# Kernel optimization log

Measured on AMD Instinct MI355X. Metric: run time of the kernel, lower is better.

The kernel has to match this reference:

```python
import jax, jax.numpy as jnp
import numpy as np

N_GRAPHS = 8
NODES_PER_G = 1024
EDGES_PER_G = 2048
N = N_GRAPHS * NODES_PER_G          # 8192 nodes
E = N_GRAPHS * EDGES_PER_G          # 16384 edges
IN_DIM, EDGE_DIM, HID, OUT_DIM, T = 10, 9, 64, 3, 5
EPS = 1e-6


def _lin(key, fan_in, fan_out):
    kw, kb = jax.random.split(key)
    s = 1.0 / np.sqrt(fan_in)
    return (jax.random.uniform(kw, (fan_in, fan_out), jnp.float32, -s, s),
            jax.random.uniform(kb, (fan_out,), jnp.float32, -s, s))


def setup_inputs() -> dict:
    key = jax.random.key(0)
    ks = jax.random.split(key, 32)
    x = jax.random.normal(ks[0], (N, IN_DIM), jnp.float32)
    edge_attr = jax.random.normal(ks[1], (E, EDGE_DIM), jnp.float32)
    # edges stay within their own graph (block structure)
    src_l = jax.random.randint(ks[2], (E,), 0, NODES_PER_G)
    dst_l = jax.random.randint(ks[3], (E,), 0, NODES_PER_G)
    off = jnp.repeat(jnp.arange(N_GRAPHS, dtype=jnp.int64) * NODES_PER_G, EDGES_PER_G)
    edge_index = jnp.stack([src_l.astype(jnp.int64) + off, dst_l.astype(jnp.int64) + off])
    batch = jnp.repeat(jnp.arange(N_GRAPHS, dtype=jnp.int64), NODES_PER_G)

    lift_w1, lift_b1 = _lin(ks[4], IN_DIM, HID)
    lift_w2, lift_b2 = _lin(ks[5], HID, HID)
    proj_w1, proj_b1 = _lin(ks[6], HID, HID)
    proj_w2, proj_b2 = _lin(ks[7], HID, OUT_DIM)

    def stackp(fn, base):
        ws, bs = zip(*[fn(ks[base + t]) for t in range(T)])
        return jnp.stack(ws), jnp.stack(bs)

    root_w, root_b = stackp(lambda k: _lin(k, HID, HID), 8)
    k_w1, k_b1 = stackp(lambda k: _lin(k, EDGE_DIM, HID), 13)
    k_w2, k_b2 = stackp(lambda k: _lin(k, HID, HID), 18)
    k_w3, k_b3 = stackp(lambda k: _lin(k, HID, HID * HID), 23)

    return dict(x=x, edge_attr=edge_attr,
                lift_w1=lift_w1, lift_b1=lift_b1, lift_w2=lift_w2, lift_b2=lift_b2,
                root_w=root_w, root_b=root_b,
                k_w1=k_w1, k_b1=k_b1, k_w2=k_w2, k_b2=k_b2, k_w3=k_w3, k_b3=k_b3,
                proj_w1=proj_w1, proj_b1=proj_b1, proj_w2=proj_w2, proj_b2=proj_b2,
                edge_index=edge_index, batch=batch)


def reference(x, edge_attr, lift_w1, lift_b1, lift_w2, lift_b2,
              root_w, root_b, k_w1, k_b1, k_w2, k_b2, k_w3, k_b3,
              proj_w1, proj_b1, proj_w2, proj_b2, edge_index, batch):
    src, dst = edge_index[0], edge_index[1]

    # --- per-graph edge_attr standardization (scatter mean/std over each graph's edges) ---
    eb = batch[src]                                           # graph id per edge [E]
    ones_e = jnp.ones((E,), jnp.float32)
    cnt = jax.ops.segment_sum(ones_e, eb, num_segments=N_GRAPHS)          # [G]
    mean = jax.ops.segment_sum(edge_attr, eb, num_segments=N_GRAPHS) / cnt[:, None]
    msq = jax.ops.segment_sum(edge_attr * edge_attr, eb, num_segments=N_GRAPHS) / cnt[:, None]
    std = jnp.sqrt(jnp.clip(msq - mean * mean, 0.0))
    ea = (edge_attr - mean[eb]) / (std[eb] + EPS)             # [E, edge_dim]

    # --- lift MLP ---
    v = jax.nn.relu(x @ lift_w1 + lift_b1) @ lift_w2 + lift_b2  # [N, HID]

    # --- T kernel layers: v' = relu(W_root v + mean_{j->i} K(e_ij) v_j) ---
    deg = jnp.clip(jax.ops.segment_sum(ones_e, dst, num_segments=N), 1.0)  # [N]
    for t in range(T):
        h = jax.nn.relu(ea @ k_w1[t] + k_b1[t])
        h = jax.nn.relu(h @ k_w2[t] + k_b2[t])
        ker = (h @ k_w3[t] + k_b3[t]).reshape(E, HID, HID)    # per-edge 64x64 kernel
        msg = jnp.einsum('eij,ej->ei', ker, v[src])           # [E, HID]
        aggr = jax.ops.segment_sum(msg, dst, num_segments=N) / deg[:, None]
        v = jax.nn.relu(v @ root_w[t] + root_b[t] + aggr)
        # dropout (p=0.1) is identity in eval mode

    # --- project MLP ---
    return jax.nn.relu(v @ proj_w1 + proj_b1) @ proj_w2 + proj_b2  # [N, OUT_DIM]
```

## Files before the change

### kernel.cpp

```cpp
#include <hip/hip_runtime.h>

#define N_GRAPHS    8
#define EDGES_PER_G 2048
#define NN          8192
#define EE          16384
#define IN_DIM      10
#define EDGE_DIM    9
#define HID         64
#define OUT_DIM     3
#define TT          5
#define EPSN        1e-6f

typedef float f32x4 __attribute__((ext_vector_type(4)));
typedef short bf16x8s __attribute__((ext_vector_type(8)));

union BF8 { __bf16 h[8]; bf16x8s v; };

__device__ inline void edgemlp16(int e0, int tid,
    const float* __restrict__ ear, const float* __restrict__ meanb,
    const float* __restrict__ invstd,
    const float* __restrict__ w1, const float* __restrict__ b1,
    const float* __restrict__ w2, const float* __restrict__ b2,
    float* smem, float* __restrict__ h2T) {
  float (*sh)[68] = (float (*)[68])smem;
  float (*st)[68] = (float (*)[68])(smem + 16 * 68);
  int g = tid >> 6, lane = tid & 63;
  int eb = e0 + g * 4;
  int gg = e0 >> 11;
  const float* mb = meanb + gg * EDGE_DIM;
  const float* is = invstd + gg * EDGE_DIM;
  float xn[4][EDGE_DIM];
#pragma unroll
  for (int k = 0; k < 4; ++k) {
    const float* er = ear + (size_t)(eb + k) * EDGE_DIM;
#pragma unroll
    for (int d = 0; d < EDGE_DIM; ++d) xn[k][d] = (er[d] - mb[d]) * is[d];
  }
  float a0 = b1[lane], a1 = a0, a2 = a0, a3 = a0;
#pragma unroll
  for (int d = 0; d < EDGE_DIM; ++d) {
    float w = w1[d * HID + lane];
    a0 += xn[0][d] * w; a1 += xn[1][d] * w;
    a2 += xn[2][d] * w; a3 += xn[3][d] * w;
  }
  sh[g * 4 + 0][lane] = fmaxf(a0, 0.f);
  sh[g * 4 + 1][lane] = fmaxf(a1, 0.f);
  sh[g * 4 + 2][lane] = fmaxf(a2, 0.f);
  sh[g * 4 + 3][lane] = fmaxf(a3, 0.f);
  __syncthreads();
  float o0 = b2[lane], o1 = o0, o2 = o0, o3 = o0;
#pragma unroll
  for (int h = 0; h < HID; ++h) {
    float w = w2[h * HID + lane];
    o0 += sh[g * 4 + 0][h] * w; o1 += sh[g * 4 + 1][h] * w;
    o2 += sh[g * 4 + 2][h] * w; o3 += sh[g * 4 + 3][h] * w;
  }
  st[g * 4 + 0][lane] = fmaxf(o0, 0.f);
  st[g * 4 + 1][lane] = fmaxf(o1, 0.f);
  st[g * 4 + 2][lane] = fmaxf(o2, 0.f);
  st[g * 4 + 3][lane] = fmaxf(o3, 0.f);
  __syncthreads();
  for (int i = tid; i < HID * 16; i += 256) {
    int c = i >> 4, eo = i & 15;
    h2T[(size_t)c * EE + e0 + eo] = st[eo][c];
  }
}

__global__ __launch_bounds__(256) void k_stats(
    const float* __restrict__ ear, float* __restrict__ meanb,
    float* __restrict__ invstd, float* __restrict__ degf) {
  __shared__ float sw[4][2 * EDGE_DIM];
  int b = blockIdx.x;
  int g = threadIdx.x >> 6, lane = threadIdx.x & 63;
  if (b < N_GRAPHS) {
    int gg = b;
    float ls[EDGE_DIM], lq[EDGE_DIM];
#pragma unroll
    for (int d = 0; d < EDGE_DIM; ++d) { ls[d] = 0.f; lq[d] = 0.f; }
    for (int e = threadIdx.x; e < EDGES_PER_G; e += blockDim.x) {
      const float* row = ear + (size_t)(gg * EDGES_PER_G + e) * EDGE_DIM;
#pragma unroll
      for (int d = 0; d < EDGE_DIM; ++d) { float xv = row[d]; ls[d] += xv; lq[d] += xv * xv; }
    }
#pragma unroll
    for (int d = 0; d < EDGE_DIM; ++d) {
#pragma unroll
      for (int off = 32; off > 0; off >>= 1) {
        ls[d] += __shfl_down(ls[d], off);
        lq[d] += __shfl_down(lq[d], off);
      }
    }
    if (lane == 0) {
#pragma unroll
      for (int d = 0; d < EDGE_DIM; ++d) {
        sw[g][d] = ls[d];
        sw[g][EDGE_DIM + d] = lq[d];
      }
    }
    __syncthreads();
    if (threadIdx.x < EDGE_DIM) {
      int d = threadIdx.x;
      float s0 = sw[0][d] + sw[1][d] + sw[2][d] + sw[3][d];
      float q0 = sw[0][EDGE_DIM + d] + sw[1][EDGE_DIM + d] +
                 sw[2][EDGE_DIM + d] + sw[3][EDGE_DIM + d];
      float m  = s0 * (1.0f / EDGES_PER_G);
      float mq = q0 * (1.0f / EDGES_PER_G);
      float var = fmaxf(mq - m * m, 0.f);
      meanb[gg * EDGE_DIM + d]  = m;
      invstd[gg * EDGE_DIM + d] = 1.f / (sqrtf(var) + EPSN);
    }
  } else {
    int idx = (b - N_GRAPHS) * 256 + threadIdx.x;
    ((float4*)degf)[idx] = make_float4(0.f, 0.f, 0.f, 0.f);
  }
}

#define PRE_EM0   (EE / 16)
#define PRE_LIFT  (NN / 4)
#define PRE_BPREP 1024
#define PRE_DEG   (EE / 256)
#define PRE_ZAG   (NN * HID / 1024)
__global__ __launch_bounds__(256) void k_pre(
    const float* __restrict__ x,
    const float* __restrict__ lw1, const float* __restrict__ lb1,
    const float* __restrict__ lw2, const float* __restrict__ lb2,
    float* __restrict__ v,
    const float* __restrict__ kw3, const float* __restrict__ kb3,
    unsigned short* __restrict__ Bbf,
    const int* __restrict__ dst, float* __restrict__ degf,
    const float* __restrict__ ear, const float* __restrict__ meanb,
    const float* __restrict__ invstd, float* __restrict__ aggr,
    const float* __restrict__ w1, const float* __restrict__ b1,
    const float* __restrict__ w2, const float* __restrict__ b2,
    float* __restrict__ h2T0) {
  __shared__ float smem[2 * 16 * 68];
  int b = blockIdx.x;
  int g = threadIdx.x >> 6, lane = threadIdx.x & 63;
  if (b < PRE_EM0) {
    edgemlp16(b * 16, threadIdx.x, ear, meanb, invstd, w1, b1, w2, b2,
              smem, h2T0);
  } else if (b < PRE_EM0 + PRE_LIFT) {
    float (*sh)[HID] = (float (*)[HID])smem;
    int n = (b - PRE_EM0) * 4 + g;
    const float* xr = x + n * IN_DIM;
    float a = lb1[lane];
#pragma unroll
    for (int d = 0; d < IN_DIM; ++d) a += xr[d] * lw1[d * HID + lane];
    sh[g][lane] = fmaxf(a, 0.f);
    __syncthreads();
    float o = lb2[lane];
#pragma unroll
    for (int h = 0; h < HID; ++h) o += sh[g][h] * lw2[h * HID + lane];
    v[n * HID + lane] = o;
  } else if (b < PRE_EM0 + PRE_LIFT + PRE_BPREP) {
    const int total = TT * 65 * 4096;
    for (int i = (b - (PRE_EM0 + PRE_LIFT)) * 256 + (int)threadIdx.x; i < total;
         i += PRE_BPREP * 256) {
      int xx   = i & 4095;
      int call = i >> 12;
      int t = call / 65;
      int c = call - t * 65;
      int sn = xx >> 9;
      int s  = sn >> 2, nt = sn & 3;
      int l9 = xx & 511;
      int ln = l9 >> 3, jj = l9 & 7;
      int nn15 = ln & 15, qq = ln >> 4;
      int x_in = (nt * 16 + nn15) * 64 + s * 32 + qq * 8 + jj;
      float val = (c < 64) ? kw3[(size_t)(t * 64 + c) * 4096 + x_in]
                           : kb3[(size_t)t * 4096 + x_in];
      union { __bf16 h; unsigned short s16; } u;
      u.h = (__bf16)val;
      Bbf[i] = u.s16;
    }
  } else if (b < PRE_EM0 + PRE_LIFT + PRE_BPREP + PRE_DEG) {
    int e = (b - (PRE_EM0 + PRE_LIFT + PRE_BPREP)) * 256 + threadIdx.x;
    atomicAdd(&degf[dst[e]], 1.f);
  } else {
    int idx = (b - (PRE_EM0 + PRE_LIFT + PRE_BPREP + PRE_DEG)) * 256 + threadIdx.x;
    ((float4*)aggr)[idx] = make_float4(0.f, 0.f, 0.f, 0.f);
  }
}

__global__ __launch_bounds__(256) void k_msg(const float* __restrict__ v,
    const float* __restrict__ h2T_r, const unsigned short* __restrict__ Bt,
    const int* __restrict__ src, const int* __restrict__ dst,
    float* __restrict__ aggr, int nEm,
    const float* __restrict__ ear, const float* __restrict__ meanb,
    const float* __restrict__ invstd,
    const float* __restrict__ w1, const float* __restrict__ b1,
    const float* __restrict__ w2, const float* __restrict__ b2,
    float* __restrict__ h2T_w) {
  __shared__ float smem[2 * 16 * 68];
  int b = blockIdx.x;
  if (b < 512) {
    int kchunk = b & 3;
    int ebb    = (b >> 2) * 128;
    int w    = threadIdx.x >> 6;
    int lane = threadIdx.x & 63;
    int n15  = lane & 15;
    int q    = lane >> 4;
    int ebase = ebb + w * 32;

    bf16x8s ubf[2][2];
#pragma unroll
    for (int mt = 0; mt < 2; ++mt) {
      int e = ebase + mt * 16 + n15;
      const float4* vr = (const float4*)(v + (size_t)src[e] * HID);
      int f0 = q * 2;
#pragma unroll
      for (int s = 0; s < 2; ++s) {
        float4 pa = vr[s * 8 + f0], pb = vr[s * 8 + f0 + 1];
        BF8 u;
        u.h[0] = (__bf16)pa.x; u.h[1] = (__bf16)pa.y;
        u.h[2] = (__bf16)pa.z; u.h[3] = (__bf16)pa.w;
        u.h[4] = (__bf16)pb.x; u.h[5] = (__bf16)pb.y;
        u.h[6] = (__bf16)pb.z; u.h[7] = (__bf16)pb.w;
        ubf[mt][s] = u.v;
      }
    }

    f32x4 acc[2][4];
#pragma unroll
    for (int mt = 0; mt < 2; ++mt)
#pragma unroll
      for (int nt = 0; nt < 4; ++nt) acc[mt][nt] = (f32x4)0.0f;

    int c0 = kchunk * 16;
    const unsigned short* Bp = Bt + (size_t)c0 * 4096 + lane * 8;
    const float* hq = h2T_r + (size_t)c0 * EE + ebase + q * 4;

#pragma unroll 4
    for (int cc = 0; cc < 16; ++cc) {
      const unsigned short* Bc = Bp + (size_t)cc * 4096;
      bf16x8s bfr[2][4];
#pragma unroll
      for (int s = 0; s < 2; ++s)
#pragma unroll
        for (int nt = 0; nt < 4; ++nt)
          bfr[s][nt] = *(const bf16x8s*)(Bc + (s * 4 + nt) * 512);
      float4 h4[2];
      h4[0] = *(const float4*)(hq + (size_t)cc * EE);
      h4[1] = *(const float4*)(hq + (size_t)cc * EE + 16);
#pragma unroll
      for (int mt = 0; mt < 2; ++mt) {
        f32x4 tmp[4];
#pragma unroll
        for (int nt = 0; nt < 4; ++nt) {
          f32x4 t0 = __builtin_amdgcn_mfma_f32_16x16x32_bf16(
              ubf[mt][0], bfr[0][nt], (f32x4)0.0f, 0, 0, 0);
          tmp[nt] = __builtin_amdgcn_mfma_f32_16x16x32_bf16(
              ubf[mt][1], bfr[1][nt], t0, 0, 0, 0);
        }
        float4 hh = h4[mt];
#pragma unroll
        for (int nt = 0; nt < 4; ++nt) {
          acc[mt][nt][0] += hh.x * tmp[nt][0];
          acc[mt][nt][1] += hh.y * tmp[nt][1];
          acc[mt][nt][2] += hh.z * tmp[nt][2];
          acc[mt][nt][3] += hh.w * tmp[nt][3];
        }
      }
    }

    if (kchunk == 3) {
      const unsigned short* Bc = Bt + (size_t)64 * 4096 + lane * 8;
      bf16x8s bfr[2][4];
#pragma unroll
      for (int s = 0; s < 2; ++s)
#pragma unroll
        for (int nt = 0; nt < 4; ++nt)
          bfr[s][nt] = *(const bf16x8s*)(Bc + (s * 4 + nt) * 512);
#pragma unroll
      for (int s = 0; s < 2; ++s)
#pragma unroll
        for (int mt = 0; mt < 2; ++mt)
#pragma unroll
          for (int nt = 0; nt < 4; ++nt)
            acc[mt][nt] = __builtin_amdgcn_mfma_f32_16x16x32_bf16(
                ubf[mt][s], bfr[s][nt], acc[mt][nt], 0, 0, 0);
    }

#pragma unroll
    for (int mt = 0; mt < 2; ++mt) {
#pragma unroll
      for (int r = 0; r < 4; ++r) {
        int e = ebase + mt * 16 + q * 4 + r;
        int d = dst[e];
        float* ag = aggr + (size_t)d * HID;
#pragma unroll
        for (int nt = 0; nt < 4; ++nt)
          atomicAdd(ag + nt * 16 + n15, acc[mt][nt][r]);
      }
    }
  } else if (b < 512 + nEm) {
    edgemlp16((b - 512) * 16, threadIdx.x, ear, meanb, invstd,
              w1, b1, w2, b2, smem, h2T_w);
  }
}

__global__ __launch_bounds__(256) void k_upd(
    float* __restrict__ v, const float* __restrict__ rw, const float* __restrict__ rb,
    float* __restrict__ aggr, const float* __restrict__ degf) {
  __shared__ float sh[4][HID];
  int g = threadIdx.x >> 6, lane = threadIdx.x & 63;
  int n = blockIdx.x * 4 + g;
  int idx = n * HID + lane;
  sh[g][lane] = v[idx];
  __syncthreads();
  float inv = 1.f / fmaxf(degf[n], 1.f);
  float o = rb[lane] + aggr[idx] * inv;
  aggr[idx] = 0.f;
#pragma unroll
  for (int h = 0; h < HID; ++h) o += sh[g][h] * rw[h * HID + lane];
  v[idx] = fmaxf(o, 0.f);
}

__global__ __launch_bounds__(256) void k_upd_proj(
    const float* __restrict__ v, const float* __restrict__ rw,
    const float* __restrict__ rb,
    const float* __restrict__ aggr, const float* __restrict__ degf,
    const float* __restrict__ pw1, const float* __restrict__ pb1,
    const float* __restrict__ pw2, const float* __restrict__ pb2,
    float* __restrict__ out) {
  __shared__ float sh[4][HID];
  int g = threadIdx.x >> 6, lane = threadIdx.x & 63;
  int n = blockIdx.x * 4 + g;
  int idx = n * HID + lane;
  sh[g][lane] = v[idx];
  __syncthreads();
  float inv = 1.f / fmaxf(degf[n], 1.f);
  float o = rb[lane] + aggr[idx] * inv;
#pragma unroll
  for (int h = 0; h < HID; ++h) o += sh[g][h] * rw[h * HID + lane];
  float vn = fmaxf(o, 0.f);
  __syncthreads();
  sh[g][lane] = vn;
  __syncthreads();
  float a = pb1[lane];
#pragma unroll
  for (int h = 0; h < HID; ++h) a += sh[g][h] * pw1[h * HID + lane];
  float h1 = fmaxf(a, 0.f);
  __syncthreads();
  sh[g][lane] = h1;
  __syncthreads();
  if (lane < OUT_DIM) {
    float oo = pb2[lane];
#pragma unroll
    for (int h = 0; h < HID; ++h) oo += sh[g][h] * pw2[h * OUT_DIM + lane];
    out[n * OUT_DIM + lane] = oo;
  }
}

extern "C" void kernel_launch(void* const* d_in, const int* in_sizes, int n_in,
                              void* d_out, int out_size, void* d_ws, size_t ws_size,
                              hipStream_t stream) {
  const float* x        = (const float*)d_in[0];
  const float* ear      = (const float*)d_in[1];
  const float* lift_w1  = (const float*)d_in[2];
  const float* lift_b1  = (const float*)d_in[3];
  const float* lift_w2  = (const float*)d_in[4];
  const float* lift_b2  = (const float*)d_in[5];
  const float* root_w   = (const float*)d_in[6];
  const float* root_b   = (const float*)d_in[7];
  const float* kw1      = (const float*)d_in[8];
  const float* kb1      = (const float*)d_in[9];
  const float* kw2      = (const float*)d_in[10];
  const float* kb2      = (const float*)d_in[11];
  const float* kw3      = (const float*)d_in[12];
  const float* kb3      = (const float*)d_in[13];
  const float* pw1      = (const float*)d_in[14];
  const float* pb1      = (const float*)d_in[15];
  const float* pw2      = (const float*)d_in[16];
  const float* pb2      = (const float*)d_in[17];
  const int* edge_index = (const int*)d_in[18];
  const int* src = edge_index;
  const int* dst = edge_index + EE;
  float* out = (float*)d_out;

  float* ws     = (float*)d_ws;
  float* aggr   = ws;
  float* degf   = aggr + NN * HID;
  float* h2Ta   = degf + NN;
  float* h2Tb   = h2Ta + (size_t)HID * EE;
  float* vbuf   = h2Tb + (size_t)HID * EE;
  float* meanb  = vbuf + NN * HID;
  float* invstd = meanb + 72;
  unsigned short* Bbf = (unsigned short*)(invstd + 72);

  k_stats<<<2 * N_GRAPHS, 256, 0, stream>>>(ear, meanb, invstd, degf);

  const int PRE_BLOCKS = PRE_EM0 + PRE_LIFT + PRE_BPREP + PRE_DEG + PRE_ZAG;
  k_pre<<<PRE_BLOCKS, 256, 0, stream>>>(
      x, lift_w1, lift_b1, lift_w2, lift_b2, vbuf, kw3, kb3, Bbf,
      dst, degf, ear, meanb, invstd, aggr,
      kw1, kb1, kw2, kb2, h2Ta);

  for (int t = 0; t < TT; ++t) {
    const float* hr = (t & 1) ? h2Tb : h2Ta;
    float*       hw = (t & 1) ? h2Ta : h2Tb;
    int nEm = (t < TT - 1) ? EE / 16 : 0;
    int tt  = (t < TT - 1) ? t + 1 : t;
    k_msg<<<512 + nEm, 256, 0, stream>>>(
        vbuf, hr, Bbf + (size_t)t * 65 * 4096, src, dst, aggr, nEm,
        ear, meanb, invstd,
        kw1 + (size_t)tt * EDGE_DIM * HID, kb1 + (size_t)tt * HID,
        kw2 + (size_t)tt * HID * HID, kb2 + (size_t)tt * HID, hw);
    if (t < TT - 1) {
      k_upd<<<NN / 4, 256, 0, stream>>>(
          vbuf, root_w + (size_t)t * HID * HID, root_b + (size_t)t * HID,
          aggr, degf);
    } else {
      k_upd_proj<<<NN / 4, 256, 0, stream>>>(
          vbuf, root_w + (size_t)t * HID * HID, root_b + (size_t)t * HID,
          aggr, degf, pw1, pb1, pw2, pb2, out);
    }
  }
}
```

Baseline: 379.1 us.

## Double-buffer per-edge kernel weight tiles into LDS via async global_load_lds

In the message kernel, each wave used to load the bf16 B weight tiles straight from global memory into registers on every iteration. The new code stages each 4096-element tile cooperatively into a double-buffered LDS array using global_load_lds, prefetching the next tile while the current one is consumed. The bias tile handled by kchunk 3 is folded into the same loop as a 17th iteration. This removes the 4x redundant global loads across waves and overlaps loading with compute, at the cost of a full barrier and vmcnt(0) wait every iteration. The vmcnt(0) wait also serializes the h2T loads.

```diff
diff --git a/kernel.cpp b/kernel.cpp
--- a/kernel.cpp
+++ b/kernel.cpp
@@ -15,6 +15,12 @@
 typedef short bf16x8s __attribute__((ext_vector_type(8)));
 
 union BF8 { __bf16 h[8]; bf16x8s v; };
+
+__device__ inline void gl_lds16(const unsigned short* g, unsigned short* l) {
+  __builtin_amdgcn_global_load_lds(
+      (const __attribute__((address_space(1))) unsigned int*)g,
+      (__attribute__((address_space(3))) unsigned int*)l, 16, 0, 0);
+}
 
 __device__ inline void edgemlp16(int e0, int tid,
     const float* __restrict__ ear, const float* __restrict__ meanb,
@@ -190,7 +196,7 @@
     const float* __restrict__ w1, const float* __restrict__ b1,
     const float* __restrict__ w2, const float* __restrict__ b2,
     float* __restrict__ h2T_w) {
-  __shared__ float smem[2 * 16 * 68];
+  __shared__ unsigned short bstage[2][4096];
   int b = blockIdx.x;
   if (b < 512) {
     int kchunk = b & 3;
@@ -226,58 +232,70 @@
       for (int nt = 0; nt < 4; ++nt) acc[mt][nt] = (f32x4)0.0f;
 
     int c0 = kchunk * 16;
-    const unsigned short* Bp = Bt + (size_t)c0 * 4096 + lane * 8;
     const float* hq = h2T_r + (size_t)c0 * EE + ebase + q * 4;
-
-#pragma unroll 4
-    for (int cc = 0; cc < 16; ++cc) {
-      const unsigned short* Bc = Bp + (size_t)cc * 4096;
+    const int NCC = (kchunk == 3) ? 17 : 16;
+
+    auto stage = [&](int cc, int cur) {
+      const unsigned short* gt = (cc < 16)
+          ? Bt + (size_t)(c0 + cc) * 4096
+          : Bt + (size_t)64 * 4096;
+      const unsigned short* gsrc = gt + w * 1024 + lane * 8;
+      unsigned short* ldst = &bstage[cur][w * 1024];
+      gl_lds16(gsrc, ldst);
+      gl_lds16(gsrc + 512, ldst + 512);
+    };
+
+    stage(0, 0);
+    asm volatile("s_waitcnt vmcnt(0)" ::: "memory");
+    __builtin_amdgcn_s_barrier();
+
+    int cur = 0;
+    for (int cc = 0; cc < NCC; ++cc) {
+      if (cc + 1 < NCC) stage(cc + 1, cur ^ 1);
+      __builtin_amdgcn_sched_barrier(0);
+      const unsigned short* Bs = &bstage[cur][lane * 8];
       bf16x8s bfr[2][4];
 #pragma unroll
       for (int s = 0; s < 2; ++s)
 #pragma unroll
         for (int nt = 0; nt < 4; ++nt)
-          bfr[s][nt] = *(const bf16x8s*)(Bc + (s * 4 + nt) * 512);
-      float4 h4[2];
-      h4[0] = *(const float4*)(hq + (size_t)cc * EE);
-      h4[1] = *(const float4*)(hq + (size_t)cc * EE + 16);
-#pragma unroll
-      for (int mt = 0; mt < 2; ++mt) {
-        f32x4 tmp[4];
-#pragma unroll
-        for (int nt = 0; nt < 4; ++nt) {
-          f32x4 t0 = __builtin_amdgcn_mfma_f32_16x16x32_bf16(
-              ubf[mt][0], bfr[0][nt], (f32x4)0.0f, 0, 0, 0);
-          tmp[nt] = __builtin_amdgcn_mfma_f32_16x16x32_bf16(
-              ubf[mt][1], bfr[1][nt], t0, 0, 0, 0);
+          bfr[s][nt] = *(const bf16x8s*)(Bs + (s * 4 + nt) * 512);
+      if (cc < 16) {
+        float4 h4[2];
+        h4[0] = *(const float4*)(hq + (size_t)cc * EE);
+        h4[1] = *(const float4*)(hq + (size_t)cc * EE + 16);
+#pragma unroll
+        for (int mt = 0; mt < 2; ++mt) {
+          f32x4 tmp[4];
+#pragma unroll
+          for (int nt = 0; nt < 4; ++nt) {
+            f32x4 t0 = __builtin_amdgcn_mfma_f32_16x16x32_bf16(
+                ubf[mt][0], bfr[0][nt], (f32x4)0.0f, 0, 0, 0);
+            tmp[nt] = __builtin_amdgcn_mfma_f32_16x16x32_bf16(
+                ubf[mt][1], bfr[1][nt], t0, 0, 0, 0);
+          }
+          float4 hh = h4[mt];
+#pragma unroll
+          for (int nt = 0; nt < 4; ++nt) {
+            acc[mt][nt][0] += hh.x * tmp[nt][0];
+            acc[mt][nt][1] += hh.y * tmp[nt][1];
+            acc[mt][nt][2] += hh.z * tmp[nt][2];
+            acc[mt][nt][3] += hh.w * tmp[nt][3];
+          }
         }
-        float4 hh = h4[mt];
-#pragma unroll
-        for (int nt = 0; nt < 4; ++nt) {
-          acc[mt][nt][0] += hh.x * tmp[nt][0];
-          acc[mt][nt][1] += hh.y * tmp[nt][1];
-          acc[mt][nt][2] += hh.z * tmp[nt][2];
-          acc[mt][nt][3] += hh.w * tmp[nt][3];
-        }
+      } else {
+#pragma unroll
+        for (int s = 0; s < 2; ++s)
+#pragma unroll
+          for (int mt = 0; mt < 2; ++mt)
+#pragma unroll
+            for (int nt = 0; nt < 4; ++nt)
+              acc[mt][nt] = __builtin_amdgcn_mfma_f32_16x16x32_bf16(
+                  ubf[mt][s], bfr[s][nt], acc[mt][nt], 0, 0, 0);
       }
-    }
-
-    if (kchunk == 3) {
-      const unsigned short* Bc = Bt + (size_t)64 * 4096 + lane * 8;
-      bf16x8s bfr[2][4];
-#pragma unroll
-      for (int s = 0; s < 2; ++s)
-#pragma unroll
-        for (int nt = 0; nt < 4; ++nt)
-          bfr[s][nt] = *(const bf16x8s*)(Bc + (s * 4 + nt) * 512);
-#pragma unroll
-      for (int s = 0; s < 2; ++s)
-#pragma unroll
-        for (int mt = 0; mt < 2; ++mt)
-#pragma unroll
-          for (int nt = 0; nt < 4; ++nt)
-            acc[mt][nt] = __builtin_amdgcn_mfma_f32_16x16x32_bf16(
-                ubf[mt][s], bfr[s][nt], acc[mt][nt], 0, 0, 0);
+      asm volatile("s_waitcnt vmcnt(0)" ::: "memory");
+      __builtin_amdgcn_s_barrier();
+      cur ^= 1;
     }
 
 #pragma unroll
@@ -294,7 +312,7 @@
     }
   } else if (b < 512 + nEm) {
     edgemlp16((b - 512) * 16, threadIdx.x, ear, meanb, invstd,
-              w1, b1, w2, b2, smem, h2T_w);
+              w1, b1, w2, b2, (float*)bstage, h2T_w);
   }
 }
 
```

Result: faster. 340.5 us (-10.2%).
